# Kernel optimization log

Hardware: AMD Instinct MI355X
Metric: run time of the kernel (lower is better)

Reference implementation:

```python
import jax, jax.numpy as jnp
import numpy as np
import math

HEADS = 8
HIDDEN = 512
HEAD_DIM = HIDDEN // HEADS
BATCH = 16
N = 512
ALPHA = 1.0 / math.sqrt(HEAD_DIM)


def setup_inputs() -> dict:
    key = jax.random.key(0)
    ks = jax.random.split(key, 6)
    stdv_qkv = 1.0 / math.sqrt(HEAD_DIM)
    stdv_o = 1.0 / math.sqrt(HIDDEN)
    return {
        "x": jax.random.normal(ks[0], (BATCH, N, HIDDEN), dtype=jnp.float32),
        "edge": jax.random.normal(ks[1], (HEADS, BATCH, N, N), dtype=jnp.float32),
        "Wq": jax.random.uniform(ks[2], (HEADS, HIDDEN, HEAD_DIM), jnp.float32, -stdv_qkv, stdv_qkv),
        "Wk": jax.random.uniform(ks[3], (HEADS, HIDDEN, HEAD_DIM), jnp.float32, -stdv_qkv, stdv_qkv),
        "Wv": jax.random.uniform(ks[4], (HEADS, HIDDEN, HEAD_DIM), jnp.float32, -stdv_qkv, stdv_qkv),
        "Wo": jax.random.uniform(ks[5], (HIDDEN, HIDDEN), jnp.float32, -stdv_o, stdv_o),
    }


def reference(x, edge, Wq, Wk, Wv, Wo):
    # per-head projections: x [b,n,h] x W [g,h,d] -> [g,b,n,d]
    Q = jnp.einsum("bnh,ghd->gbnd", x, Wq)
    K = jnp.einsum("bnh,ghd->gbnd", x, Wk)
    V = jnp.einsum("bnh,ghd->gbnd", x, Wv)
    # edge-biased attention scores [g,b,n,n]
    S = edge + ALPHA * jnp.einsum("gbnd,gbmd->gbnm", Q, K)
    S = jax.nn.softmax(S, axis=-1)
    # attend and merge heads: [g,b,n,d] -> [b,n,g*d]
    o = jnp.einsum("gbnm,gbmd->bngd", S, V)
    o = o.reshape(o.shape[0], o.shape[1], -1)
    return o @ Wo
```

## Files before the change

kernel.cpp:

```cpp
#include <hip/hip_runtime.h>

typedef __bf16 bf16;
typedef __bf16 bf16x4 __attribute__((ext_vector_type(4)));
typedef __bf16 bf16x8 __attribute__((ext_vector_type(8)));
typedef float f32x4 __attribute__((ext_vector_type(4)));

#define ALPHA_ 0.125f


__device__ __forceinline__ void gload16(const void* g, void* l) {
  __builtin_amdgcn_global_load_lds((__attribute__((address_space(1))) void*)(g),
                                   (__attribute__((address_space(3))) void*)(l),
                                   16, 0, 0);
}

__global__ void cast_x_kernel(const float* __restrict__ x, bf16* __restrict__ xb) {
  int i = blockIdx.x * 256 + threadIdx.x;
  float4 v = ((const float4*)x)[i];
  bf16x4 o = {(bf16)v.x, (bf16)v.y, (bf16)v.z, (bf16)v.w};
  ((bf16x4*)xb)[i] = o;
}

__global__ void prep_w_kernel(const float* __restrict__ Wq, const float* __restrict__ Wk,
                              const float* __restrict__ Wv, bf16* __restrict__ wcat) {
  int i = blockIdx.x * 256 + threadIdx.x;
  int h = i & 511, j = i >> 9;
  int qkv = j >> 9, g = (j >> 6) & 7, d = j & 63;
  const float* W = (qkv == 0) ? Wq : ((qkv == 1) ? Wk : Wv);
  wcat[i] = (bf16)W[((g << 9) + h) * 64 + d];
}

__global__ void prep_wo_kernel(const float* __restrict__ Wo, bf16* __restrict__ wot) {
  int i = blockIdx.x * 256 + threadIdx.x;
  int k = i & 511, n = i >> 9;
  wot[i] = (bf16)Wo[(k << 9) + n];
}

template <int RM, int RN, int MODE>
__global__ __launch_bounds__(256, 2) void gemm2_kernel(
    const bf16* __restrict__ A, const bf16* __restrict__ Bt, int Kdim, int Ndim,
    float* __restrict__ Cf, bf16* __restrict__ Qo, bf16* __restrict__ Ko,
    bf16* __restrict__ Vto) {
  constexpr int BM = RM * 64, BN = RN * 64;
  constexpr int MI = BM / 32, NJ = BN / 32;
  __shared__ bf16 lA[2][BM * 32];
  __shared__ bf16 lB[2][BN * 32];
  const int t = threadIdx.x;
  const int w = t >> 6;
  const int lane = t & 63;
  const int lhi = lane >> 4, llo = lane & 15;
  const int m0 = blockIdx.y * BM, n0 = blockIdx.x * BN;
  const int wr = (w >> 1) * (BM / 2), wc = (w & 1) * (BN / 2);

  f32x4 acc[MI][NJ] = {};
  const int nkt = Kdim >> 5;

  auto stage = [&](int buf, int kt) {
#pragma unroll
    for (int c = 0; c < RM; ++c) {
      int u = c * 256 + t;
      gload16(A + (size_t)(m0 + (u >> 2)) * Kdim + kt * 32 + (u & 3) * 8,
              &lA[buf][c * 2048 + w * 512]);
    }
#pragma unroll
    for (int c = 0; c < RN; ++c) {
      int u = c * 256 + t;
      gload16(Bt + (size_t)(n0 + (u >> 2)) * Kdim + kt * 32 + (u & 3) * 8,
              &lB[buf][c * 2048 + w * 512]);
    }
  };

  stage(0, 0);
  asm volatile("s_waitcnt vmcnt(0)" ::: "memory");
  __builtin_amdgcn_s_barrier();
  __builtin_amdgcn_sched_barrier(0);

  for (int kt = 0; kt < nkt; ++kt) {
    const int cur = kt & 1;
    if (kt + 1 < nkt) stage(cur ^ 1, kt + 1);
    __builtin_amdgcn_sched_barrier(0);

    bf16x8 af[MI], bfr[NJ];
#pragma unroll
    for (int i = 0; i < MI; ++i)
      af[i] = *(const bf16x8*)&lA[cur][(wr + i * 16 + llo) * 32 + lhi * 8];
#pragma unroll
    for (int j = 0; j < NJ; ++j)
      bfr[j] = *(const bf16x8*)&lB[cur][(wc + j * 16 + llo) * 32 + lhi * 8];
#pragma unroll
    for (int i = 0; i < MI; ++i)
#pragma unroll
      for (int j = 0; j < NJ; ++j)
        acc[i][j] = __builtin_amdgcn_mfma_f32_16x16x32_bf16(af[i], bfr[j], acc[i][j], 0, 0, 0);

    __builtin_amdgcn_sched_barrier(0);
    asm volatile("s_waitcnt vmcnt(0)" ::: "memory");
    __builtin_amdgcn_s_barrier();
    __builtin_amdgcn_sched_barrier(0);
  }

#pragma unroll
  for (int i = 0; i < MI; ++i) {
    int row = m0 + wr + i * 16 + lhi * 4;
#pragma unroll
    for (int j = 0; j < NJ; ++j) {
      int col = n0 + wc + j * 16 + llo;
#pragma unroll
      for (int r = 0; r < 4; ++r) {
        float v = acc[i][j][r];
        int rr = row + r;
        if (MODE == 0) {
          int qkv = col >> 9, g = (col >> 6) & 7, d = col & 63;
          bf16 bv = (bf16)v;
          if (qkv == 0)
            Qo[((size_t)g * 8192 + rr) * 64 + d] = bv;
          else if (qkv == 1)
            Ko[((size_t)g * 8192 + rr) * 64 + d] = bv;
          else {
            int b = rr >> 9, n = rr & 511;
            Vto[(((size_t)g * 16 + b) * 64 + d) * 512 + n] = bv;
          }
        } else {
          Cf[(size_t)rr * Ndim + col] = v;
        }
      }
    }
  }
}

__global__ __launch_bounds__(256, 4) void attn_kernel(
    const bf16* __restrict__ Qa, const bf16* __restrict__ Ka,
    const bf16* __restrict__ Vta, const float* __restrict__ edge,
    bf16* __restrict__ Oatt) {
  __shared__ bf16 lK[2][64 * 64];
  __shared__ bf16 lV[2][64 * 64];
  const int t = threadIdx.x, w = t >> 6, lane = t & 63;
  const int lhi = lane >> 4, llo = lane & 15;
  const int qt = blockIdx.x, b = blockIdx.y, g = blockIdx.z;
  const int q0 = qt * 64 + w * 16;
  const bf16* Qg = Qa + ((size_t)g * 8192 + b * 512) * 64;
  const bf16* Kg = Ka + ((size_t)g * 8192 + b * 512) * 64;
  const bf16* Vg = Vta + ((size_t)g * 16 + b) * (64 * 512);
  const float* eg = edge + ((size_t)g * 16 + b) * (512 * 512);

  bf16x8 qf[2];
#pragma unroll
  for (int ks = 0; ks < 2; ++ks)
    qf[ks] = *(const bf16x8*)(Qg + (size_t)(q0 + llo) * 64 + ks * 32 + lhi * 8);

  f32x4 oacc[4] = {};
  float mrow = -3e38f, lrow = 0.f;

  const int r0 = t >> 3;
  const int r1 = r0 + 32;
  const int cs = (((t & 7) ^ (r0 & 7)) << 3);

  f32x4 eb[2][4];

  gload16(Kg + (size_t)r0 * 64 + cs, &lK[0][w * 512]);
  gload16(Kg + (size_t)r1 * 64 + cs, &lK[0][2048 + w * 512]);
  gload16(Vg + (size_t)r0 * 512 + cs, &lV[0][w * 512]);
  gload16(Vg + (size_t)r1 * 512 + cs, &lV[0][2048 + w * 512]);
#pragma unroll
  for (int ni = 0; ni < 4; ++ni)
    eb[0][ni] = *(const f32x4*)(eg + (size_t)(q0 + llo) * 512 + ni * 16 + lhi * 4);
  __builtin_amdgcn_sched_barrier(0);

#pragma unroll
  for (int it = 0; it < 8; ++it) {
    const int cur = it & 1, nxt = cur ^ 1;
    const int kv0 = it * 64;

    if (it < 7) {
      const int kvn = kv0 + 64;
      gload16(Kg + (size_t)(kvn + r0) * 64 + cs, &lK[nxt][w * 512]);
      gload16(Kg + (size_t)(kvn + r1) * 64 + cs, &lK[nxt][2048 + w * 512]);
      gload16(Vg + (size_t)r0 * 512 + kvn + cs, &lV[nxt][w * 512]);
      gload16(Vg + (size_t)r1 * 512 + kvn + cs, &lV[nxt][2048 + w * 512]);
#pragma unroll
      for (int ni = 0; ni < 4; ++ni)
        eb[nxt][ni] = *(const f32x4*)(eg + (size_t)(q0 + llo) * 512 + kvn + ni * 16 + lhi * 4);
    }
    __builtin_amdgcn_sched_barrier(0);
    if (it < 7)
      asm volatile("s_waitcnt vmcnt(8)" ::: "memory");
    else
      asm volatile("s_waitcnt vmcnt(0)" ::: "memory");
    __builtin_amdgcn_sched_barrier(0);
    __builtin_amdgcn_s_barrier();
    __builtin_amdgcn_sched_barrier(0);

    f32x4 sc[4] = {};
    __builtin_amdgcn_s_setprio(1);
#pragma unroll
    for (int ks = 0; ks < 2; ++ks) {
      bf16x8 kf[4];
#pragma unroll
      for (int ni = 0; ni < 4; ++ni) {
        int row = ni * 16 + llo;
        kf[ni] = *(const bf16x8*)&lK[cur][(row * 64 + ks * 32 + lhi * 8) ^ ((row & 7) << 3)];
      }
#pragma unroll
      for (int ni = 0; ni < 4; ++ni)
        sc[ni] = __builtin_amdgcn_mfma_f32_16x16x32_bf16(kf[ni], qf[ks], sc[ni], 0, 0, 0);
    }
    __builtin_amdgcn_s_setprio(0);

    float mx = -3e38f;
#pragma unroll
    for (int ni = 0; ni < 4; ++ni)
#pragma unroll
      for (int r = 0; r < 4; ++r) {
        float sv = fmaf(ALPHA_, sc[ni][r], eb[cur][ni][r]);
        sc[ni][r] = sv;
        mx = fmaxf(mx, sv);
      }
    mx = fmaxf(mx, __shfl_xor(mx, 16));
    mx = fmaxf(mx, __shfl_xor(mx, 32));
    float mnew = fmaxf(mrow, mx);
    float s = __expf(mrow - mnew);
    mrow = mnew;
    float rsum = 0.f;
#pragma unroll
    for (int ni = 0; ni < 4; ++ni)
#pragma unroll
      for (int r = 0; r < 4; ++r) {
        float p = __expf(sc[ni][r] - mnew);
        sc[ni][r] = p;
        rsum += p;
      }
    rsum += __shfl_xor(rsum, 16);
    rsum += __shfl_xor(rsum, 32);
    lrow = lrow * s + rsum;

#pragma unroll
    for (int r = 0; r < 4; ++r) {
      float sq = __shfl(s, (lane & 48) | (lhi * 4 + r));
#pragma unroll
      for (int nc = 0; nc < 4; ++nc) oacc[nc][r] *= sq;
    }

    __builtin_amdgcn_s_setprio(1);
#pragma unroll
    for (int ks2 = 0; ks2 < 2; ++ks2) {
      const int n0 = ks2 * 2, n1 = n0 + 1;
      unsigned xa, xb, ya, yb;
      asm("v_cvt_pk_bf16_f32 %0, %1, %2" : "=v"(xa) : "v"(sc[n0][0]), "v"(sc[n0][1]));
      asm("v_cvt_pk_bf16_f32 %0, %1, %2" : "=v"(xb) : "v"(sc[n0][2]), "v"(sc[n0][3]));
      asm("v_cvt_pk_bf16_f32 %0, %1, %2" : "=v"(ya) : "v"(sc[n1][0]), "v"(sc[n1][1]));
      asm("v_cvt_pk_bf16_f32 %0, %1, %2" : "=v"(yb) : "v"(sc[n1][2]), "v"(sc[n1][3]));
      asm("v_permlane32_swap_b32 %0, %1" : "+v"(xa), "+v"(ya));
      asm("v_permlane16_swap_b32 %0, %1" : "+v"(xa), "+v"(ya));
      asm("v_permlane32_swap_b32 %0, %1" : "+v"(xb), "+v"(yb));
      asm("v_permlane16_swap_b32 %0, %1" : "+v"(xb), "+v"(yb));
      union { unsigned wd[4]; bf16x8 v; } fu;
      fu.wd[0] = xa; fu.wd[1] = xb; fu.wd[2] = ya; fu.wd[3] = yb;
      bf16x8 pf = fu.v;

      bf16x8 vf[4];
#pragma unroll
      for (int nc = 0; nc < 4; ++nc) {
        int row = nc * 16 + llo;
        vf[nc] = *(const bf16x8*)&lV[cur][(row * 64 + ks2 * 32 + lhi * 8) ^ ((row & 7) << 3)];
      }
#pragma unroll
      for (int nc = 0; nc < 4; ++nc)
        oacc[nc] = __builtin_amdgcn_mfma_f32_16x16x32_bf16(pf, vf[nc], oacc[nc], 0, 0, 0);
    }
    __builtin_amdgcn_s_setprio(0);

    if (it < 7) {
      __builtin_amdgcn_sched_barrier(0);
      __builtin_amdgcn_s_barrier();
      __builtin_amdgcn_sched_barrier(0);
    }
  }

  float rcpl = 1.0f / lrow;
#pragma unroll
  for (int r = 0; r < 4; ++r) {
    float lr = __shfl(rcpl, (lane & 48) | (lhi * 4 + r));
    int qrow = q0 + lhi * 4 + r;
#pragma unroll
    for (int nc = 0; nc < 4; ++nc) {
      float ov = oacc[nc][r] * lr;
      Oatt[((size_t)b * 512 + qrow) * 512 + g * 64 + nc * 16 + llo] = (bf16)ov;
    }
  }
}

extern "C" void kernel_launch(void* const* d_in, const int* in_sizes, int n_in,
                              void* d_out, int out_size, void* d_ws, size_t ws_size,
                              hipStream_t stream) {
  (void)in_sizes; (void)n_in; (void)out_size; (void)ws_size;
  const float* x = (const float*)d_in[0];
  const float* edge = (const float*)d_in[1];
  const float* Wq = (const float*)d_in[2];
  const float* Wk = (const float*)d_in[3];
  const float* Wv = (const float*)d_in[4];
  const float* Wo = (const float*)d_in[5];
  float* out = (float*)d_out;

  char* ws = (char*)d_ws;
  bf16* xb   = (bf16*)(ws + 0);
  bf16* wcat = (bf16*)(ws + 8388608);
  bf16* wot  = (bf16*)(ws + 9961472);
  bf16* Qa   = (bf16*)(ws + 10485760);
  bf16* Ka   = (bf16*)(ws + 18874368);
  bf16* Vta  = (bf16*)(ws + 27262976);
  bf16* Oatt = (bf16*)(ws + 35651584);

  cast_x_kernel<<<4096, 256, 0, stream>>>(x, xb);
  prep_w_kernel<<<3072, 256, 0, stream>>>(Wq, Wk, Wv, wcat);
  prep_wo_kernel<<<1024, 256, 0, stream>>>(Wo, wot);

  gemm2_kernel<2, 2, 0><<<dim3(12, 64), 256, 0, stream>>>(xb, wcat, 512, 1536,
                                                          nullptr, Qa, Ka, Vta);
  attn_kernel<<<dim3(8, 16, 8), 256, 0, stream>>>(Qa, Ka, Vta, edge, Oatt);
  gemm2_kernel<2, 1, 1><<<dim3(8, 64), 256, 0, stream>>>(Oatt, wot, 512, 512,
                                                         out, nullptr, nullptr, nullptr);
}
```

Baseline: 108.7 us.

## Load K/V fragments directly from global into registers, drop LDS staging

The attention kernel no longer stages K and V tiles through double-buffered shared memory with block barriers. Each wave now loads its own K, V and edge fragments straight from global memory into registers, working through 32-key steps over 16 iterations with software prefetch of the next step. This removes the LDS round trips and workgroup barriers. In exchange the four waves in a block each fetch the same K/V data separately, raising global/L2 traffic, and load latency is hidden only by register prefetch and occupancy.

```diff
diff --git a/kernel.cpp b/kernel.cpp
--- a/kernel.cpp
+++ b/kernel.cpp
@@ -132,17 +132,19 @@
     const bf16* __restrict__ Qa, const bf16* __restrict__ Ka,
     const bf16* __restrict__ Vta, const float* __restrict__ edge,
     bf16* __restrict__ Oatt) {
-  __shared__ bf16 lK[2][64 * 64];
-  __shared__ bf16 lV[2][64 * 64];
-  const int t = threadIdx.x, w = t >> 6, lane = t & 63;
+  const int t = threadIdx.x, lane = t & 63;
   const int lhi = lane >> 4, llo = lane & 15;
   const int qt = blockIdx.x, b = blockIdx.y, g = blockIdx.z;
-  const int q0 = qt * 64 + w * 16;
+  const int q0 = qt * 64 + (t >> 6) * 16;
   const bf16* Qg = Qa + ((size_t)g * 8192 + b * 512) * 64;
   const bf16* Kg = Ka + ((size_t)g * 8192 + b * 512) * 64;
   const bf16* Vg = Vta + ((size_t)g * 16 + b) * (64 * 512);
   const float* eg = edge + ((size_t)g * 16 + b) * (512 * 512);
 
+  const bf16* kbase = Kg + (size_t)llo * 64 + lhi * 8;
+  const bf16* vbase = Vg + (size_t)llo * 512 + lhi * 8;
+  const float* ebase = eg + (size_t)(q0 + llo) * 512 + lhi * 4;
+
   bf16x8 qf[2];
 #pragma unroll
   for (int ks = 0; ks < 2; ++ks)
@@ -151,70 +153,55 @@
   f32x4 oacc[4] = {};
   float mrow = -3e38f, lrow = 0.f;
 
-  const int r0 = t >> 3;
-  const int r1 = r0 + 32;
-  const int cs = (((t & 7) ^ (r0 & 7)) << 3);
-
-  f32x4 eb[2][4];
-
-  gload16(Kg + (size_t)r0 * 64 + cs, &lK[0][w * 512]);
-  gload16(Kg + (size_t)r1 * 64 + cs, &lK[0][2048 + w * 512]);
-  gload16(Vg + (size_t)r0 * 512 + cs, &lV[0][w * 512]);
-  gload16(Vg + (size_t)r1 * 512 + cs, &lV[0][2048 + w * 512]);
-#pragma unroll
-  for (int ni = 0; ni < 4; ++ni)
-    eb[0][ni] = *(const f32x4*)(eg + (size_t)(q0 + llo) * 512 + ni * 16 + lhi * 4);
-  __builtin_amdgcn_sched_barrier(0);
-
-#pragma unroll
-  for (int it = 0; it < 8; ++it) {
-    const int cur = it & 1, nxt = cur ^ 1;
-    const int kv0 = it * 64;
-
-    if (it < 7) {
-      const int kvn = kv0 + 64;
-      gload16(Kg + (size_t)(kvn + r0) * 64 + cs, &lK[nxt][w * 512]);
-      gload16(Kg + (size_t)(kvn + r1) * 64 + cs, &lK[nxt][2048 + w * 512]);
-      gload16(Vg + (size_t)r0 * 512 + kvn + cs, &lV[nxt][w * 512]);
-      gload16(Vg + (size_t)r1 * 512 + kvn + cs, &lV[nxt][2048 + w * 512]);
-#pragma unroll
-      for (int ni = 0; ni < 4; ++ni)
-        eb[nxt][ni] = *(const f32x4*)(eg + (size_t)(q0 + llo) * 512 + kvn + ni * 16 + lhi * 4);
-    }
-    __builtin_amdgcn_sched_barrier(0);
-    if (it < 7)
-      asm volatile("s_waitcnt vmcnt(8)" ::: "memory");
-    else
-      asm volatile("s_waitcnt vmcnt(0)" ::: "memory");
-    __builtin_amdgcn_sched_barrier(0);
-    __builtin_amdgcn_s_barrier();
-    __builtin_amdgcn_sched_barrier(0);
-
-    f32x4 sc[4] = {};
-    __builtin_amdgcn_s_setprio(1);
-#pragma unroll
-    for (int ks = 0; ks < 2; ++ks) {
-      bf16x8 kf[4];
-#pragma unroll
-      for (int ni = 0; ni < 4; ++ni) {
-        int row = ni * 16 + llo;
-        kf[ni] = *(const bf16x8*)&lK[cur][(row * 64 + ks * 32 + lhi * 8) ^ ((row & 7) << 3)];
-      }
-#pragma unroll
-      for (int ni = 0; ni < 4; ++ni)
-        sc[ni] = __builtin_amdgcn_mfma_f32_16x16x32_bf16(kf[ni], qf[ks], sc[ni], 0, 0, 0);
-    }
-    __builtin_amdgcn_s_setprio(0);
+  bf16x8 kf[2][2], vf[4];
+  f32x4 ef[2];
+#pragma unroll
+  for (int ks = 0; ks < 2; ++ks)
+#pragma unroll
+    for (int ni = 0; ni < 2; ++ni)
+      kf[ks][ni] = *(const bf16x8*)(kbase + ni * 1024 + ks * 32);
+#pragma unroll
+  for (int nc = 0; nc < 4; ++nc)
+    vf[nc] = *(const bf16x8*)(vbase + nc * 8192);
+#pragma unroll
+  for (int ni = 0; ni < 2; ++ni)
+    ef[ni] = *(const f32x4*)(ebase + ni * 16);
+
+#pragma unroll
+  for (int it = 0; it < 16; ++it) {
+    const int kvn = (it + 1) * 32;
+
+    f32x4 sc[2] = {};
+#pragma unroll
+    for (int ks = 0; ks < 2; ++ks)
+#pragma unroll
+      for (int ni = 0; ni < 2; ++ni)
+        sc[ni] = __builtin_amdgcn_mfma_f32_16x16x32_bf16(kf[ks][ni], qf[ks], sc[ni], 0, 0, 0);
+
+    if (it < 15) {
+#pragma unroll
+      for (int ks = 0; ks < 2; ++ks)
+#pragma unroll
+        for (int ni = 0; ni < 2; ++ni)
+          kf[ks][ni] = *(const bf16x8*)(kbase + (size_t)kvn * 64 + ni * 1024 + ks * 32);
+    }
 
     float mx = -3e38f;
 #pragma unroll
-    for (int ni = 0; ni < 4; ++ni)
+    for (int ni = 0; ni < 2; ++ni)
 #pragma unroll
       for (int r = 0; r < 4; ++r) {
-        float sv = fmaf(ALPHA_, sc[ni][r], eb[cur][ni][r]);
+        float sv = fmaf(ALPHA_, sc[ni][r], ef[ni][r]);
         sc[ni][r] = sv;
         mx = fmaxf(mx, sv);
       }
+
+    if (it < 15) {
+#pragma unroll
+      for (int ni = 0; ni < 2; ++ni)
+        ef[ni] = *(const f32x4*)(ebase + kvn + ni * 16);
+    }
+
     mx = fmaxf(mx, __shfl_xor(mx, 16));
     mx = fmaxf(mx, __shfl_xor(mx, 32));
     float mnew = fmaxf(mrow, mx);
@@ -222,7 +209,7 @@
     mrow = mnew;
     float rsum = 0.f;
 #pragma unroll
-    for (int ni = 0; ni < 4; ++ni)
+    for (int ni = 0; ni < 2; ++ni)
 #pragma unroll
       for (int r = 0; r < 4; ++r) {
         float p = __expf(sc[ni][r] - mnew);
@@ -240,15 +227,12 @@
       for (int nc = 0; nc < 4; ++nc) oacc[nc][r] *= sq;
     }
 
-    __builtin_amdgcn_s_setprio(1);
-#pragma unroll
-    for (int ks2 = 0; ks2 < 2; ++ks2) {
-      const int n0 = ks2 * 2, n1 = n0 + 1;
+    {
       unsigned xa, xb, ya, yb;
-      asm("v_cvt_pk_bf16_f32 %0, %1, %2" : "=v"(xa) : "v"(sc[n0][0]), "v"(sc[n0][1]));
-      asm("v_cvt_pk_bf16_f32 %0, %1, %2" : "=v"(xb) : "v"(sc[n0][2]), "v"(sc[n0][3]));
-      asm("v_cvt_pk_bf16_f32 %0, %1, %2" : "=v"(ya) : "v"(sc[n1][0]), "v"(sc[n1][1]));
-      asm("v_cvt_pk_bf16_f32 %0, %1, %2" : "=v"(yb) : "v"(sc[n1][2]), "v"(sc[n1][3]));
+      asm("v_cvt_pk_bf16_f32 %0, %1, %2" : "=v"(xa) : "v"(sc[0][0]), "v"(sc[0][1]));
+      asm("v_cvt_pk_bf16_f32 %0, %1, %2" : "=v"(xb) : "v"(sc[0][2]), "v"(sc[0][3]));
+      asm("v_cvt_pk_bf16_f32 %0, %1, %2" : "=v"(ya) : "v"(sc[1][0]), "v"(sc[1][1]));
+      asm("v_cvt_pk_bf16_f32 %0, %1, %2" : "=v"(yb) : "v"(sc[1][2]), "v"(sc[1][3]));
       asm("v_permlane32_swap_b32 %0, %1" : "+v"(xa), "+v"(ya));
       asm("v_permlane16_swap_b32 %0, %1" : "+v"(xa), "+v"(ya));
       asm("v_permlane32_swap_b32 %0, %1" : "+v"(xb), "+v"(yb));
@@ -256,24 +240,18 @@
       union { unsigned wd[4]; bf16x8 v; } fu;
       fu.wd[0] = xa; fu.wd[1] = xb; fu.wd[2] = ya; fu.wd[3] = yb;
       bf16x8 pf = fu.v;
-
-      bf16x8 vf[4];
-#pragma unroll
-      for (int nc = 0; nc < 4; ++nc) {
-        int row = nc * 16 + llo;
-        vf[nc] = *(const bf16x8*)&lV[cur][(row * 64 + ks2 * 32 + lhi * 8) ^ ((row & 7) << 3)];
-      }
 #pragma unroll
       for (int nc = 0; nc < 4; ++nc)
         oacc[nc] = __builtin_amdgcn_mfma_f32_16x16x32_bf16(pf, vf[nc], oacc[nc], 0, 0, 0);
     }
-    __builtin_amdgcn_s_setprio(0);
-
-    if (it < 7) {
-      __builtin_amdgcn_sched_barrier(0);
-      __builtin_amdgcn_s_barrier();
-      __builtin_amdgcn_sched_barrier(0);
-    }
+
+    if (it < 15) {
+#pragma unroll
+      for (int nc = 0; nc < 4; ++nc)
+        vf[nc] = *(const bf16x8*)(vbase + nc * 8192 + kvn);
+    }
+
+    __builtin_amdgcn_sched_barrier(0);
   }
 
   float rcpl = 1.0f / lrow;
```

Result: slower. 141.1 us (+29.8%).
